# Optimization experiments

Hardware: AMD Instinct MI355X
Metric: run time of the kernel (lower is better)

The kernel has to match this reference:

```python
import jax, jax.numpy as jnp
import numpy as np

N_NODES = 200_000  # total nodes (segment id space for the CSR-style grouped reduce)


def setup_inputs() -> dict:
    key = jax.random.key(0)
    k1, k2, k3, k4, k5 = jax.random.split(key, 5)
    E, D = 1_000_000, 128   # interaction events, message dim
    B, K = 50_000, 20       # neighbor-attention batch, neighbors per node
    node_ids = jax.random.randint(k1, (E,), 0, N_NODES, dtype=jnp.int64)
    message = jax.random.normal(k2, (E, D), dtype=jnp.float32)
    timestamps = jax.random.uniform(k3, (E, 1), dtype=jnp.float32)
    nei1 = jax.random.normal(k4, (B, K, D), dtype=jnp.float32)
    nei2 = jax.random.normal(k5, (B, K, D), dtype=jnp.float32)
    return {"node_ids": node_ids, "message": message, "timestamps": timestamps,
            "nei1": nei1, "nei2": nei2}


def reference(node_ids, message, timestamps, nei1, nei2):
    # --- merged_by_segment_csr: grouped reduction over variable-length event groups.
    # torch does sort + unique_consecutive + cumsum + segment_csr; in jax the
    # equivalent (and efficient) form is a fixed-size segment reduce keyed by node id.
    ones = jnp.ones((node_ids.shape[0],), dtype=message.dtype)
    counts = jax.ops.segment_sum(ones, node_ids, num_segments=N_NODES)          # [N]
    msg_sum = jax.ops.segment_sum(message, node_ids, num_segments=N_NODES)      # [N, D]
    # msg_agg == 'mean' (segment_csr mean); empty segments yield 0.
    merged_message = msg_sum / jnp.maximum(counts, 1.0)[:, None]
    merged_t = jax.ops.segment_max(timestamps, node_ids, num_segments=N_NODES)  # [N, 1]
    merged_t = jnp.where(counts[:, None] > 0, merged_t, jnp.zeros_like(merged_t))
    # --- NeighborAttention: matmul(node1, node2^T).sum(dim=2) -> softmax over dim 0.
    # sum_j (n1[k] . n2[j]) == n1[k] . sum_j n2[j]  (avoids the [B,K,K] intermediate)
    logits = jnp.einsum('bkd,bd->bk', nei1, nei2.sum(axis=1))                   # [B, K]
    score = jax.nn.softmax(logits, axis=0)  # softmax over dim=0, as in the module
    return (merged_message, merged_t, score)
```

## Files before the change

### kernel.cpp

```cpp
#include <hip/hip_runtime.h>

#define N_NODES 200000
#define E_EVENTS 1000000
#define D_DIM 128
#define B_BATCH 50000
#define K_NEI 20

#define SCAN_BLK 196


__global__ void hist(const int* __restrict__ ids, int* __restrict__ counts)
{
    int e = blockIdx.x * blockDim.x + threadIdx.x;
    if (e < E_EVENTS) atomicAdd(counts + ids[e], 1);
}

__global__ void scan_block(const int* __restrict__ counts, int* __restrict__ blockSums)
{
    __shared__ int sd[256];
    int t = threadIdx.x, base = blockIdx.x * 1024 + t * 4;
    int s = 0;
#pragma unroll
    for (int j = 0; j < 4; ++j) { int i = base + j; if (i < N_NODES) s += counts[i]; }
    sd[t] = s; __syncthreads();
    for (int off = 128; off; off >>= 1) {
        if (t < off) sd[t] += sd[t + off];
        __syncthreads();
    }
    if (t == 0) blockSums[blockIdx.x] = sd[0];
}

__global__ void scan_tops(int* __restrict__ blockSums)
{
    __shared__ int sd[256];
    int t = threadIdx.x;
    int v = (t < SCAN_BLK) ? blockSums[t] : 0;
    sd[t] = v; __syncthreads();
    for (int off = 1; off < 256; off <<= 1) {
        int x = (t >= off) ? sd[t - off] : 0;
        __syncthreads();
        sd[t] += x;
        __syncthreads();
    }
    if (t < SCAN_BLK) blockSums[t] = sd[t] - v;
}

__global__ void scan_final(const int* __restrict__ counts, const int* __restrict__ blockSums,
                           int* __restrict__ offsets, int* __restrict__ cursor)
{
    __shared__ int sd[256];
    int t = threadIdx.x, base = blockIdx.x * 1024 + t * 4;
    int c[4];
#pragma unroll
    for (int j = 0; j < 4; ++j) { int i = base + j; c[j] = (i < N_NODES) ? counts[i] : 0; }
    int tsum = c[0] + c[1] + c[2] + c[3];
    sd[t] = tsum; __syncthreads();
    for (int off = 1; off < 256; off <<= 1) {
        int x = (t >= off) ? sd[t - off] : 0;
        __syncthreads();
        sd[t] += x;
        __syncthreads();
    }
    int excl = sd[t] - tsum + blockSums[blockIdx.x];
#pragma unroll
    for (int j = 0; j < 4; ++j) {
        int i = base + j;
        if (i < N_NODES) { offsets[i] = excl; cursor[i] = excl; }
        excl += c[j];
    }
}

template<int TSP>
__global__ void scatter_t(const int* __restrict__ ids, const float* __restrict__ ts,
                          int* __restrict__ cursor, void* __restrict__ permv)
{
    int e = blockIdx.x * blockDim.x + threadIdx.x;
    if (e < E_EVENTS) {
        int pos = atomicAdd(cursor + ids[e], 1);
        if (TSP) ((int2*)permv)[pos] = make_int2(e, __float_as_int(ts[e]));
        else     ((int*)permv)[pos]  = e;
    }
}

template<int TSP>
__global__ void __launch_bounds__(256, 8)
seg_attn_t(const void* __restrict__ permv, const int* __restrict__ offsets,
           const float* __restrict__ message, const float* __restrict__ ts,
           const float* __restrict__ nei1, const float* __restrict__ nei2,
           float* __restrict__ msg_out, float* __restrict__ t_out,
           float* __restrict__ logits)
{
    int g = blockIdx.x / 5, r = blockIdx.x % 5;
    int wid  = threadIdx.x >> 6;
    int lane = threadIdx.x & 63;
    int c = lane & 31;
    int h = lane >> 5;

    if (r < 4) {
        int n = (g * 4 + r) * 4 + wid;
        int start = offsets[n];
        int end   = (n < N_NODES - 1) ? offsets[n + 1] : E_EVENTS;
        int len   = end - start;

        const float4* msg4 = reinterpret_cast<const float4*>(message);
        float4 acc0 = make_float4(0.f, 0.f, 0.f, 0.f);
        float4 acc1 = make_float4(0.f, 0.f, 0.f, 0.f);
        float tmax = 0.f;

        for (int base = start; base < end; base += 64) {
            int cl = min(end - base, 64);
            int e_l = 0; float t_l = 0.f;
            if (lane < cl) {
                if (TSP) {
                    int2 pe = ((const int2*)permv)[base + lane];
                    e_l = pe.x; t_l = __int_as_float(pe.y);
                } else {
                    e_l = ((const int*)permv)[base + lane];
                    t_l = ts[e_l];
                }
            }
            tmax = fmaxf(tmax, t_l);
            int i = 0;
            for (; i + 8 <= cl; i += 8) {
                int eA = __shfl(e_l, i + 0 + h);
                int eB = __shfl(e_l, i + 2 + h);
                int eC = __shfl(e_l, i + 4 + h);
                int eD = __shfl(e_l, i + 6 + h);
                float4 vA = msg4[(size_t)eA * 32 + c];
                float4 vB = msg4[(size_t)eB * 32 + c];
                float4 vC = msg4[(size_t)eC * 32 + c];
                float4 vD = msg4[(size_t)eD * 32 + c];
                acc0.x += vA.x; acc0.y += vA.y; acc0.z += vA.z; acc0.w += vA.w;
                acc1.x += vB.x; acc1.y += vB.y; acc1.z += vB.z; acc1.w += vB.w;
                acc0.x += vC.x; acc0.y += vC.y; acc0.z += vC.z; acc0.w += vC.w;
                acc1.x += vD.x; acc1.y += vD.y; acc1.z += vD.z; acc1.w += vD.w;
            }
            for (; i + 2 <= cl; i += 2) {
                int e = __shfl(e_l, i + h);
                float4 v = msg4[(size_t)e * 32 + c];
                acc0.x += v.x; acc0.y += v.y; acc0.z += v.z; acc0.w += v.w;
            }
            if (i < cl) {
                int e = __shfl(e_l, i);
                if (h == 0) {
                    float4 v = msg4[(size_t)e * 32 + c];
                    acc0.x += v.x; acc0.y += v.y; acc0.z += v.z; acc0.w += v.w;
                }
            }
        }
        float4 acc = make_float4(acc0.x + acc1.x, acc0.y + acc1.y,
                                 acc0.z + acc1.z, acc0.w + acc1.w);
        acc.x += __shfl_xor(acc.x, 32);
        acc.y += __shfl_xor(acc.y, 32);
        acc.z += __shfl_xor(acc.z, 32);
        acc.w += __shfl_xor(acc.w, 32);
        float inv = 1.0f / (float)max(len, 1);
        if (h == 0) {
            reinterpret_cast<float4*>(msg_out)[(size_t)n * 32 + c] =
                make_float4(acc.x * inv, acc.y * inv, acc.z * inv, acc.w * inv);
        }
#pragma unroll
        for (int off = 32; off; off >>= 1) tmax = fmaxf(tmax, __shfl_xor(tmax, off));
        if (lane == 0) t_out[n] = tmax;
    } else {
        int b = g * 4 + wid;
        const float4* n2 = reinterpret_cast<const float4*>(nei2) + (size_t)b * (K_NEI * 32);
        float4 acc = make_float4(0.f, 0.f, 0.f, 0.f);
#pragma unroll
        for (int i = 0; i < K_NEI / 2; ++i) {
            float4 v = n2[(2 * i + h) * 32 + c];
            acc.x += v.x; acc.y += v.y; acc.z += v.z; acc.w += v.w;
        }
        float4 s4;
        s4.x = acc.x + __shfl_xor(acc.x, 32);
        s4.y = acc.y + __shfl_xor(acc.y, 32);
        s4.z = acc.z + __shfl_xor(acc.z, 32);
        s4.w = acc.w + __shfl_xor(acc.w, 32);

        const float4* n1 = reinterpret_cast<const float4*>(nei1) + (size_t)b * (K_NEI * 32);
        float p[K_NEI / 2];
#pragma unroll
        for (int i = 0; i < K_NEI / 2; ++i) {
            float4 v = n1[(2 * i + h) * 32 + c];
            float pp = v.x * s4.x + v.y * s4.y + v.z * s4.z + v.w * s4.w;
#pragma unroll
            for (int off = 16; off; off >>= 1) pp += __shfl_xor(pp, off);
            p[i] = pp;
        }
        int sel = c >> 1;
        float v = p[0];
#pragma unroll
        for (int i = 1; i < K_NEI / 2; ++i) v = (sel == i) ? p[i] : v;
        float vf = __shfl(v, ((lane & 1) << 5) + c);
        if (lane < K_NEI) logits[(size_t)b * K_NEI + lane] = vf;
    }
}

__global__ void softmax_partial(const float* __restrict__ logits, float2* __restrict__ partials)
{
    int t = threadIdx.x;
    float m[K_NEI], s[K_NEI];
#pragma unroll
    for (int k = 0; k < K_NEI; ++k) { m[k] = -INFINITY; s[k] = 0.f; }

    for (int b = blockIdx.x * 256 + t; b < B_BATCH; b += 128 * 256) {
        const float4* row = reinterpret_cast<const float4*>(logits + (size_t)b * K_NEI);
        float v[K_NEI];
#pragma unroll
        for (int q = 0; q < 5; ++q) {
            float4 rr = row[q];
            v[q * 4 + 0] = rr.x; v[q * 4 + 1] = rr.y; v[q * 4 + 2] = rr.z; v[q * 4 + 3] = rr.w;
        }
#pragma unroll
        for (int k = 0; k < K_NEI; ++k) {
            float nm = fmaxf(m[k], v[k]);
            s[k] = s[k] * expf(m[k] - nm) + expf(v[k] - nm);
            m[k] = nm;
        }
    }
#pragma unroll
    for (int k = 0; k < K_NEI; ++k) {
#pragma unroll
        for (int off = 32; off; off >>= 1) {
            float om = __shfl_xor(m[k], off);
            float os = __shfl_xor(s[k], off);
            float nm = fmaxf(m[k], om);
            s[k] = s[k] * expf(m[k] - nm) + os * expf(om - nm);
            m[k] = nm;
        }
    }
    __shared__ float lm[4][K_NEI], lsum[4][K_NEI];
    int wid = t >> 6, lane = t & 63;
    if (lane == 0) {
#pragma unroll
        for (int k = 0; k < K_NEI; ++k) { lm[wid][k] = m[k]; lsum[wid][k] = s[k]; }
    }
    __syncthreads();
    if (t < K_NEI) {
        float mm = lm[0][t], ss = lsum[0][t];
#pragma unroll
        for (int w = 1; w < 4; ++w) {
            float om = lm[w][t], os = lsum[w][t];
            float nm = fmaxf(mm, om);
            ss = ss * expf(mm - nm) + os * expf(om - nm);
            mm = nm;
        }
        partials[blockIdx.x * K_NEI + t] = make_float2(mm, ss);
    }
}

__global__ void softmax_final(const float2* __restrict__ partials, float2* __restrict__ stats)
{
    int t = threadIdx.x;
    if (t < K_NEI) {
        float mm = -INFINITY, ss = 0.f;
        for (int i = 0; i < 128; ++i) {
            float2 p = partials[i * K_NEI + t];
            float nm = fmaxf(mm, p.x);
            ss = ss * expf(mm - nm) + p.y * expf(p.x - nm);
            mm = nm;
        }
        stats[t] = make_float2(mm, ss);
    }
}

__global__ void softmax_norm(float* __restrict__ score, const float2* __restrict__ stats)
{
    int i = blockIdx.x * blockDim.x + threadIdx.x;
    if (i >= B_BATCH * K_NEI) return;
    int k = i % K_NEI;
    float2 st = stats[k];
    score[i] = expf(score[i] - st.x) / st.y;
}

extern "C" void kernel_launch(void* const* d_in, const int* in_sizes, int n_in,
                              void* d_out, int out_size, void* d_ws, size_t ws_size,
                              hipStream_t stream)
{
    const int*   node_ids = (const int*)  d_in[0];
    const float* message  = (const float*)d_in[1];
    const float* ts       = (const float*)d_in[2];
    const float* nei1     = (const float*)d_in[3];
    const float* nei2     = (const float*)d_in[4];

    float* out     = (float*)d_out;
    float* msg_out = out;
    float* t_out   = out + (size_t)N_NODES * D_DIM;
    float* score   = t_out + N_NODES;

    int*    wsi       = (int*)d_ws;
    int*    counts    = wsi;
    int*    offsets   = wsi + 200000;
    int*    cursor    = wsi + 400000;
    int*    blockSums = wsi + 600000;
    float2* stats     = (float2*)(wsi + 600256);
    float2* partials  = (float2*)(wsi + 600320);
    void*   permv     = (void*)(wsi + 605440);

    bool tsp = ws_size >= ((size_t)605440 * 4 + (size_t)E_EVENTS * 8);

    hipMemsetAsync(counts, 0, (size_t)N_NODES * sizeof(int), stream);

    hist<<<(E_EVENTS + 255) / 256, 256, 0, stream>>>(node_ids, counts);
    scan_block<<<SCAN_BLK, 256, 0, stream>>>(counts, blockSums);
    scan_tops<<<1, 256, 0, stream>>>(blockSums);
    scan_final<<<SCAN_BLK, 256, 0, stream>>>(counts, blockSums, offsets, cursor);

    if (tsp) {
        scatter_t<1><<<(E_EVENTS + 255) / 256, 256, 0, stream>>>(node_ids, ts, cursor, permv);
        seg_attn_t<1><<<12500 * 5, 256, 0, stream>>>(
            permv, offsets, message, ts, nei1, nei2, msg_out, t_out, score);
    } else {
        scatter_t<0><<<(E_EVENTS + 255) / 256, 256, 0, stream>>>(node_ids, ts, cursor, permv);
        seg_attn_t<0><<<12500 * 5, 256, 0, stream>>>(
            permv, offsets, message, ts, nei1, nei2, msg_out, t_out, score);
    }

    softmax_partial<<<128, 256, 0, stream>>>(score, partials);
    softmax_final<<<1, 64, 0, stream>>>(partials, stats);
    softmax_norm<<<(B_BATCH * K_NEI + 255) / 256, 256, 0, stream>>>(score, stats);
}
```

Baseline: 472.4 us.

## Fuse all stages into one persistent kernel with grid barriers

Replaces the chain of nine kernel launches with one persistent kernel sized to device occupancy. The stages (histogram, scan, scatter, segment reduce, attention, softmax) are separated by atomic grid-wide barriers. Part of the attention work now overlaps the scatter phase, and the segment-reduce and attention units are interleaved. This removes launch gaps and tail effects, but the grid barriers require every block to be co-resident, which risks a deadlock if occupancy is overestimated, and the fixed grid lowers parallelism in the memory-heavy phases.

```diff
diff --git a/kernel.cpp b/kernel.cpp
--- a/kernel.cpp
+++ b/kernel.cpp
@@ -6,271 +6,329 @@
 #define B_BATCH 50000
 #define K_NEI 20
 
-#define SCAN_BLK 196
-
-
-__global__ void hist(const int* __restrict__ ids, int* __restrict__ counts)
-{
-    int e = blockIdx.x * blockDim.x + threadIdx.x;
-    if (e < E_EVENTS) atomicAdd(counts + ids[e], 1);
-}
-
-__global__ void scan_block(const int* __restrict__ counts, int* __restrict__ blockSums)
-{
-    __shared__ int sd[256];
-    int t = threadIdx.x, base = blockIdx.x * 1024 + t * 4;
-    int s = 0;
-#pragma unroll
-    for (int j = 0; j < 4; ++j) { int i = base + j; if (i < N_NODES) s += counts[i]; }
-    sd[t] = s; __syncthreads();
-    for (int off = 128; off; off >>= 1) {
-        if (t < off) sd[t] += sd[t + off];
-        __syncthreads();
-    }
-    if (t == 0) blockSums[blockIdx.x] = sd[0];
-}
-
-__global__ void scan_tops(int* __restrict__ blockSums)
-{
-    __shared__ int sd[256];
-    int t = threadIdx.x;
-    int v = (t < SCAN_BLK) ? blockSums[t] : 0;
-    sd[t] = v; __syncthreads();
-    for (int off = 1; off < 256; off <<= 1) {
-        int x = (t >= off) ? sd[t - off] : 0;
-        __syncthreads();
-        sd[t] += x;
-        __syncthreads();
-    }
-    if (t < SCAN_BLK) blockSums[t] = sd[t] - v;
-}
-
-__global__ void scan_final(const int* __restrict__ counts, const int* __restrict__ blockSums,
-                           int* __restrict__ offsets, int* __restrict__ cursor)
-{
-    __shared__ int sd[256];
-    int t = threadIdx.x, base = blockIdx.x * 1024 + t * 4;
-    int c[4];
-#pragma unroll
-    for (int j = 0; j < 4; ++j) { int i = base + j; c[j] = (i < N_NODES) ? counts[i] : 0; }
-    int tsum = c[0] + c[1] + c[2] + c[3];
-    sd[t] = tsum; __syncthreads();
-    for (int off = 1; off < 256; off <<= 1) {
-        int x = (t >= off) ? sd[t - off] : 0;
-        __syncthreads();
-        sd[t] += x;
-        __syncthreads();
-    }
-    int excl = sd[t] - tsum + blockSums[blockIdx.x];
-#pragma unroll
-    for (int j = 0; j < 4; ++j) {
-        int i = base + j;
-        if (i < N_NODES) { offsets[i] = excl; cursor[i] = excl; }
-        excl += c[j];
-    }
+#define NCHUNK 196
+#define ATTN_UNITS 12500
+#define SEG_UNITS 50000
+#define ATTN_P4 2000
+
+#define WS_COUNTS   0
+#define WS_OFFSETS  200000
+#define WS_CURSOR   400000
+#define WS_CHUNK    600000
+#define WS_PARTIALS 600320
+#define WS_BARS     608256
+#define WS_PERM     608512
+
+__device__ __forceinline__ void gbar(int* bars, int idx, int G)
+{
+    __syncthreads();
+    if (threadIdx.x == 0) {
+        __threadfence();
+        __hip_atomic_fetch_add(&bars[idx * 16], 1, __ATOMIC_RELEASE,
+                               __HIP_MEMORY_SCOPE_AGENT);
+        while (__hip_atomic_load(&bars[idx * 16], __ATOMIC_ACQUIRE,
+                                 __HIP_MEMORY_SCOPE_AGENT) < G)
+            __builtin_amdgcn_s_sleep(4);
+    }
+    __syncthreads();
+}
+
+__device__ __forceinline__ void attn_unit(int u, int wid, int lane,
+    const float* __restrict__ nei1, const float* __restrict__ nei2,
+    float* __restrict__ logits)
+{
+    int b = u * 4 + wid;
+    int c = lane & 31, h = lane >> 5;
+    const float4* n2 = reinterpret_cast<const float4*>(nei2) + (size_t)b * (K_NEI * 32);
+    float4 acc = make_float4(0.f, 0.f, 0.f, 0.f);
+#pragma unroll
+    for (int i = 0; i < K_NEI / 2; ++i) {
+        float4 v = n2[(2 * i + h) * 32 + c];
+        acc.x += v.x; acc.y += v.y; acc.z += v.z; acc.w += v.w;
+    }
+    float4 s4;
+    s4.x = acc.x + __shfl_xor(acc.x, 32);
+    s4.y = acc.y + __shfl_xor(acc.y, 32);
+    s4.z = acc.z + __shfl_xor(acc.z, 32);
+    s4.w = acc.w + __shfl_xor(acc.w, 32);
+
+    const float4* n1 = reinterpret_cast<const float4*>(nei1) + (size_t)b * (K_NEI * 32);
+    float p[K_NEI / 2];
+#pragma unroll
+    for (int i = 0; i < K_NEI / 2; ++i) {
+        float4 v = n1[(2 * i + h) * 32 + c];
+        float pp = v.x * s4.x + v.y * s4.y + v.z * s4.z + v.w * s4.w;
+#pragma unroll
+        for (int off = 16; off; off >>= 1) pp += __shfl_xor(pp, off);
+        p[i] = pp;
+    }
+    int sel = c >> 1;
+    float v = p[0];
+#pragma unroll
+    for (int i = 1; i < K_NEI / 2; ++i) v = (sel == i) ? p[i] : v;
+    float vf = __shfl(v, ((lane & 1) << 5) + c);
+    if (lane < K_NEI) logits[(size_t)b * K_NEI + lane] = vf;
 }
 
 template<int TSP>
-__global__ void scatter_t(const int* __restrict__ ids, const float* __restrict__ ts,
-                          int* __restrict__ cursor, void* __restrict__ permv)
-{
-    int e = blockIdx.x * blockDim.x + threadIdx.x;
-    if (e < E_EVENTS) {
-        int pos = atomicAdd(cursor + ids[e], 1);
-        if (TSP) ((int2*)permv)[pos] = make_int2(e, __float_as_int(ts[e]));
-        else     ((int*)permv)[pos]  = e;
-    }
+__device__ __forceinline__ void seg_node(int n, int lane,
+    const void* __restrict__ permv, const int* __restrict__ offsets,
+    const float* __restrict__ message, const float* __restrict__ ts,
+    float* __restrict__ msg_out, float* __restrict__ t_out)
+{
+    int c = lane & 31, h = lane >> 5;
+    int start = offsets[n];
+    int end   = (n < N_NODES - 1) ? offsets[n + 1] : E_EVENTS;
+    int len   = end - start;
+
+    const float4* msg4 = reinterpret_cast<const float4*>(message);
+    float4 acc0 = make_float4(0.f, 0.f, 0.f, 0.f);
+    float4 acc1 = make_float4(0.f, 0.f, 0.f, 0.f);
+    float tmax = 0.f;
+
+    for (int base = start; base < end; base += 64) {
+        int cl = min(end - base, 64);
+        int e_l = 0; float t_l = 0.f;
+        if (lane < cl) {
+            if (TSP) {
+                int2 pe = ((const int2*)permv)[base + lane];
+                e_l = pe.x; t_l = __int_as_float(pe.y);
+            } else {
+                e_l = ((const int*)permv)[base + lane];
+                t_l = ts[e_l];
+            }
+        }
+        tmax = fmaxf(tmax, t_l);
+        int i = 0;
+        for (; i + 8 <= cl; i += 8) {
+            int eA = __shfl(e_l, i + 0 + h);
+            int eB = __shfl(e_l, i + 2 + h);
+            int eC = __shfl(e_l, i + 4 + h);
+            int eD = __shfl(e_l, i + 6 + h);
+            float4 vA = msg4[(size_t)eA * 32 + c];
+            float4 vB = msg4[(size_t)eB * 32 + c];
+            float4 vC = msg4[(size_t)eC * 32 + c];
+            float4 vD = msg4[(size_t)eD * 32 + c];
+            acc0.x += vA.x; acc0.y += vA.y; acc0.z += vA.z; acc0.w += vA.w;
+            acc1.x += vB.x; acc1.y += vB.y; acc1.z += vB.z; acc1.w += vB.w;
+            acc0.x += vC.x; acc0.y += vC.y; acc0.z += vC.z; acc0.w += vC.w;
+            acc1.x += vD.x; acc1.y += vD.y; acc1.z += vD.z; acc1.w += vD.w;
+        }
+        for (; i + 2 <= cl; i += 2) {
+            int e = __shfl(e_l, i + h);
+            float4 v = msg4[(size_t)e * 32 + c];
+            acc0.x += v.x; acc0.y += v.y; acc0.z += v.z; acc0.w += v.w;
+        }
+        if (i < cl) {
+            int e = __shfl(e_l, i);
+            if (h == 0) {
+                float4 v = msg4[(size_t)e * 32 + c];
+                acc0.x += v.x; acc0.y += v.y; acc0.z += v.z; acc0.w += v.w;
+            }
+        }
+    }
+    float4 acc = make_float4(acc0.x + acc1.x, acc0.y + acc1.y,
+                             acc0.z + acc1.z, acc0.w + acc1.w);
+    acc.x += __shfl_xor(acc.x, 32);
+    acc.y += __shfl_xor(acc.y, 32);
+    acc.z += __shfl_xor(acc.z, 32);
+    acc.w += __shfl_xor(acc.w, 32);
+    float inv = 1.0f / (float)max(len, 1);
+    if (h == 0) {
+        reinterpret_cast<float4*>(msg_out)[(size_t)n * 32 + c] =
+            make_float4(acc.x * inv, acc.y * inv, acc.z * inv, acc.w * inv);
+    }
+#pragma unroll
+    for (int off = 32; off; off >>= 1) tmax = fmaxf(tmax, __shfl_xor(tmax, off));
+    if (lane == 0) t_out[n] = tmax;
 }
 
 template<int TSP>
 __global__ void __launch_bounds__(256, 8)
-seg_attn_t(const void* __restrict__ permv, const int* __restrict__ offsets,
-           const float* __restrict__ message, const float* __restrict__ ts,
-           const float* __restrict__ nei1, const float* __restrict__ nei2,
-           float* __restrict__ msg_out, float* __restrict__ t_out,
-           float* __restrict__ logits)
-{
-    int g = blockIdx.x / 5, r = blockIdx.x % 5;
-    int wid  = threadIdx.x >> 6;
-    int lane = threadIdx.x & 63;
-    int c = lane & 31;
-    int h = lane >> 5;
-
-    if (r < 4) {
-        int n = (g * 4 + r) * 4 + wid;
-        int start = offsets[n];
-        int end   = (n < N_NODES - 1) ? offsets[n + 1] : E_EVENTS;
-        int len   = end - start;
-
-        const float4* msg4 = reinterpret_cast<const float4*>(message);
-        float4 acc0 = make_float4(0.f, 0.f, 0.f, 0.f);
-        float4 acc1 = make_float4(0.f, 0.f, 0.f, 0.f);
-        float tmax = 0.f;
-
-        for (int base = start; base < end; base += 64) {
-            int cl = min(end - base, 64);
-            int e_l = 0; float t_l = 0.f;
-            if (lane < cl) {
-                if (TSP) {
-                    int2 pe = ((const int2*)permv)[base + lane];
-                    e_l = pe.x; t_l = __int_as_float(pe.y);
-                } else {
-                    e_l = ((const int*)permv)[base + lane];
-                    t_l = ts[e_l];
-                }
-            }
-            tmax = fmaxf(tmax, t_l);
-            int i = 0;
-            for (; i + 8 <= cl; i += 8) {
-                int eA = __shfl(e_l, i + 0 + h);
-                int eB = __shfl(e_l, i + 2 + h);
-                int eC = __shfl(e_l, i + 4 + h);
-                int eD = __shfl(e_l, i + 6 + h);
-                float4 vA = msg4[(size_t)eA * 32 + c];
-                float4 vB = msg4[(size_t)eB * 32 + c];
-                float4 vC = msg4[(size_t)eC * 32 + c];
-                float4 vD = msg4[(size_t)eD * 32 + c];
-                acc0.x += vA.x; acc0.y += vA.y; acc0.z += vA.z; acc0.w += vA.w;
-                acc1.x += vB.x; acc1.y += vB.y; acc1.z += vB.z; acc1.w += vB.w;
-                acc0.x += vC.x; acc0.y += vC.y; acc0.z += vC.z; acc0.w += vC.w;
-                acc1.x += vD.x; acc1.y += vD.y; acc1.z += vD.z; acc1.w += vD.w;
-            }
-            for (; i + 2 <= cl; i += 2) {
-                int e = __shfl(e_l, i + h);
-                float4 v = msg4[(size_t)e * 32 + c];
-                acc0.x += v.x; acc0.y += v.y; acc0.z += v.z; acc0.w += v.w;
-            }
-            if (i < cl) {
-                int e = __shfl(e_l, i);
-                if (h == 0) {
-                    float4 v = msg4[(size_t)e * 32 + c];
-                    acc0.x += v.x; acc0.y += v.y; acc0.z += v.z; acc0.w += v.w;
-                }
-            }
-        }
-        float4 acc = make_float4(acc0.x + acc1.x, acc0.y + acc1.y,
-                                 acc0.z + acc1.z, acc0.w + acc1.w);
-        acc.x += __shfl_xor(acc.x, 32);
-        acc.y += __shfl_xor(acc.y, 32);
-        acc.z += __shfl_xor(acc.z, 32);
-        acc.w += __shfl_xor(acc.w, 32);
-        float inv = 1.0f / (float)max(len, 1);
-        if (h == 0) {
-            reinterpret_cast<float4*>(msg_out)[(size_t)n * 32 + c] =
-                make_float4(acc.x * inv, acc.y * inv, acc.z * inv, acc.w * inv);
-        }
-#pragma unroll
-        for (int off = 32; off; off >>= 1) tmax = fmaxf(tmax, __shfl_xor(tmax, off));
-        if (lane == 0) t_out[n] = tmax;
-    } else {
-        int b = g * 4 + wid;
-        const float4* n2 = reinterpret_cast<const float4*>(nei2) + (size_t)b * (K_NEI * 32);
-        float4 acc = make_float4(0.f, 0.f, 0.f, 0.f);
-#pragma unroll
-        for (int i = 0; i < K_NEI / 2; ++i) {
-            float4 v = n2[(2 * i + h) * 32 + c];
-            acc.x += v.x; acc.y += v.y; acc.z += v.z; acc.w += v.w;
-        }
-        float4 s4;
-        s4.x = acc.x + __shfl_xor(acc.x, 32);
-        s4.y = acc.y + __shfl_xor(acc.y, 32);
-        s4.z = acc.z + __shfl_xor(acc.z, 32);
-        s4.w = acc.w + __shfl_xor(acc.w, 32);
-
-        const float4* n1 = reinterpret_cast<const float4*>(nei1) + (size_t)b * (K_NEI * 32);
-        float p[K_NEI / 2];
-#pragma unroll
-        for (int i = 0; i < K_NEI / 2; ++i) {
-            float4 v = n1[(2 * i + h) * 32 + c];
-            float pp = v.x * s4.x + v.y * s4.y + v.z * s4.z + v.w * s4.w;
-#pragma unroll
-            for (int off = 16; off; off >>= 1) pp += __shfl_xor(pp, off);
-            p[i] = pp;
-        }
-        int sel = c >> 1;
-        float v = p[0];
-#pragma unroll
-        for (int i = 1; i < K_NEI / 2; ++i) v = (sel == i) ? p[i] : v;
-        float vf = __shfl(v, ((lane & 1) << 5) + c);
-        if (lane < K_NEI) logits[(size_t)b * K_NEI + lane] = vf;
-    }
-}
-
-__global__ void softmax_partial(const float* __restrict__ logits, float2* __restrict__ partials)
-{
-    int t = threadIdx.x;
-    float m[K_NEI], s[K_NEI];
-#pragma unroll
-    for (int k = 0; k < K_NEI; ++k) { m[k] = -INFINITY; s[k] = 0.f; }
-
-    for (int b = blockIdx.x * 256 + t; b < B_BATCH; b += 128 * 256) {
-        const float4* row = reinterpret_cast<const float4*>(logits + (size_t)b * K_NEI);
+mega(const int* __restrict__ ids, const float* __restrict__ message,
+     const float* __restrict__ ts,
+     const float* __restrict__ nei1, const float* __restrict__ nei2,
+     float* __restrict__ msg_out, float* __restrict__ t_out,
+     float* __restrict__ score, int* __restrict__ wsi, int G)
+{
+    int bid = blockIdx.x, t = threadIdx.x;
+    int wid = t >> 6, lane = t & 63;
+
+    int*    counts    = wsi + WS_COUNTS;
+    int*    offsets   = wsi + WS_OFFSETS;
+    int*    cursor    = wsi + WS_CURSOR;
+    int*    chunkSums = wsi + WS_CHUNK;
+    float2* partials  = (float2*)(wsi + WS_PARTIALS);
+    int*    bars      = wsi + WS_BARS;
+    void*   permv     = (void*)(wsi + WS_PERM);
+
+    __shared__ float smemf[512];
+    __shared__ int   smemi[256];
+    __shared__ float stm[K_NEI], sinv[K_NEI];
+
+    for (int e = bid * 256 + t; e < E_EVENTS; e += G * 256)
+        atomicAdd(counts + ids[e], 1);
+    gbar(bars, 0, G);
+
+    for (int cu = bid; cu < NCHUNK; cu += G) {
+        int base = cu * 1024 + t * 4, s = 0;
+#pragma unroll
+        for (int j = 0; j < 4; ++j) { int i = base + j; if (i < N_NODES) s += counts[i]; }
+        smemi[t] = s; __syncthreads();
+        for (int off = 128; off; off >>= 1) {
+            if (t < off) smemi[t] += smemi[t + off];
+            __syncthreads();
+        }
+        if (t == 0) chunkSums[cu] = smemi[0];
+        __syncthreads();
+    }
+    gbar(bars, 1, G);
+
+    if (bid == 0) {
+        int v = (t < NCHUNK) ? chunkSums[t] : 0;
+        smemi[t] = v; __syncthreads();
+        for (int off = 1; off < 256; off <<= 1) {
+            int x = (t >= off) ? smemi[t - off] : 0;
+            __syncthreads();
+            smemi[t] += x;
+            __syncthreads();
+        }
+        if (t < NCHUNK) chunkSums[t] = smemi[t] - v;
+    }
+    gbar(bars, 2, G);
+
+    for (int cu = bid; cu < NCHUNK; cu += G) {
+        int base = cu * 1024 + t * 4;
+        int c0 = (base + 0 < N_NODES) ? counts[base + 0] : 0;
+        int c1 = (base + 1 < N_NODES) ? counts[base + 1] : 0;
+        int c2 = (base + 2 < N_NODES) ? counts[base + 2] : 0;
+        int c3 = (base + 3 < N_NODES) ? counts[base + 3] : 0;
+        int tsum = c0 + c1 + c2 + c3;
+        smemi[t] = tsum; __syncthreads();
+        for (int off = 1; off < 256; off <<= 1) {
+            int x = (t >= off) ? smemi[t - off] : 0;
+            __syncthreads();
+            smemi[t] += x;
+            __syncthreads();
+        }
+        int excl = smemi[t] - tsum + chunkSums[cu];
+        if (base + 0 < N_NODES) { offsets[base + 0] = excl; cursor[base + 0] = excl; } excl += c0;
+        if (base + 1 < N_NODES) { offsets[base + 1] = excl; cursor[base + 1] = excl; } excl += c1;
+        if (base + 2 < N_NODES) { offsets[base + 2] = excl; cursor[base + 2] = excl; } excl += c2;
+        if (base + 3 < N_NODES) { offsets[base + 3] = excl; cursor[base + 3] = excl; } excl += c3;
+        __syncthreads();
+    }
+    gbar(bars, 3, G);
+
+    {
+        int Gs = G >> 1;
+        if (bid < Gs) {
+            for (int e = bid * 256 + t; e < E_EVENTS; e += Gs * 256) {
+                int pos = atomicAdd(cursor + ids[e], 1);
+                if (TSP) ((int2*)permv)[pos] = make_int2(e, __float_as_int(ts[e]));
+                else     ((int*)permv)[pos]  = e;
+            }
+        } else {
+            for (int u = bid - Gs; u < ATTN_P4; u += G - Gs)
+                attn_unit(u, wid, lane, nei1, nei2, score);
+        }
+    }
+    gbar(bars, 4, G);
+
+    for (int v = bid; v < 63000; v += G) {
+        int q = v / 6, r = v % 6;
+        if (r < 5) {
+            int s = q * 5 + r;
+            if (s < SEG_UNITS)
+                seg_node<TSP>(s * 4 + wid, lane, permv, offsets, message, ts,
+                              msg_out, t_out);
+        } else {
+            int a = ATTN_P4 + q;
+            if (a < ATTN_UNITS)
+                attn_unit(a, wid, lane, nei1, nei2, score);
+        }
+    }
+    gbar(bars, 5, G);
+
+    if (bid < NCHUNK) {
+        int b = bid * 256 + t;
+        bool val = (b < B_BATCH);
         float v[K_NEI];
-#pragma unroll
-        for (int q = 0; q < 5; ++q) {
-            float4 rr = row[q];
-            v[q * 4 + 0] = rr.x; v[q * 4 + 1] = rr.y; v[q * 4 + 2] = rr.z; v[q * 4 + 3] = rr.w;
+        if (val) {
+            const float4* row = reinterpret_cast<const float4*>(score + (size_t)b * K_NEI);
+#pragma unroll
+            for (int q = 0; q < 5; ++q) {
+                float4 r4 = row[q];
+                v[q * 4 + 0] = r4.x; v[q * 4 + 1] = r4.y;
+                v[q * 4 + 2] = r4.z; v[q * 4 + 3] = r4.w;
+            }
+        } else {
+#pragma unroll
+            for (int k = 0; k < K_NEI; ++k) v[k] = -INFINITY;
         }
 #pragma unroll
         for (int k = 0; k < K_NEI; ++k) {
-            float nm = fmaxf(m[k], v[k]);
-            s[k] = s[k] * expf(m[k] - nm) + expf(v[k] - nm);
-            m[k] = nm;
-        }
-    }
-#pragma unroll
-    for (int k = 0; k < K_NEI; ++k) {
-#pragma unroll
-        for (int off = 32; off; off >>= 1) {
-            float om = __shfl_xor(m[k], off);
-            float os = __shfl_xor(s[k], off);
-            float nm = fmaxf(m[k], om);
-            s[k] = s[k] * expf(m[k] - nm) + os * expf(om - nm);
-            m[k] = nm;
-        }
-    }
-    __shared__ float lm[4][K_NEI], lsum[4][K_NEI];
-    int wid = t >> 6, lane = t & 63;
-    if (lane == 0) {
-#pragma unroll
-        for (int k = 0; k < K_NEI; ++k) { lm[wid][k] = m[k]; lsum[wid][k] = s[k]; }
-    }
-    __syncthreads();
-    if (t < K_NEI) {
-        float mm = lm[0][t], ss = lsum[0][t];
-#pragma unroll
-        for (int w = 1; w < 4; ++w) {
-            float om = lm[w][t], os = lsum[w][t];
-            float nm = fmaxf(mm, om);
-            ss = ss * expf(mm - nm) + os * expf(om - nm);
-            mm = nm;
-        }
-        partials[blockIdx.x * K_NEI + t] = make_float2(mm, ss);
-    }
-}
-
-__global__ void softmax_final(const float2* __restrict__ partials, float2* __restrict__ stats)
-{
-    int t = threadIdx.x;
-    if (t < K_NEI) {
-        float mm = -INFINITY, ss = 0.f;
-        for (int i = 0; i < 128; ++i) {
-            float2 p = partials[i * K_NEI + t];
-            float nm = fmaxf(mm, p.x);
-            ss = ss * expf(mm - nm) + p.y * expf(p.x - nm);
-            mm = nm;
-        }
-        stats[t] = make_float2(mm, ss);
-    }
-}
-
-__global__ void softmax_norm(float* __restrict__ score, const float2* __restrict__ stats)
-{
-    int i = blockIdx.x * blockDim.x + threadIdx.x;
-    if (i >= B_BATCH * K_NEI) return;
-    int k = i % K_NEI;
-    float2 st = stats[k];
-    score[i] = expf(score[i] - st.x) / st.y;
+            float m = v[k];
+#pragma unroll
+            for (int off = 32; off; off >>= 1) m = fmaxf(m, __shfl_xor(m, off));
+            if (lane == 0) smemf[wid * K_NEI + k] = m;
+        }
+        __syncthreads();
+        float bmx[K_NEI];
+#pragma unroll
+        for (int k = 0; k < K_NEI; ++k)
+            bmx[k] = fmaxf(fmaxf(smemf[k], smemf[K_NEI + k]),
+                           fmaxf(smemf[2 * K_NEI + k], smemf[3 * K_NEI + k]));
+#pragma unroll
+        for (int k = 0; k < K_NEI; ++k) {
+            float e = val ? expf(v[k] - bmx[k]) : 0.f;
+#pragma unroll
+            for (int off = 32; off; off >>= 1) e += __shfl_xor(e, off);
+            if (lane == 0) smemf[128 + wid * K_NEI + k] = e;
+        }
+        __syncthreads();
+        if (t < K_NEI) {
+            float m4 = fmaxf(fmaxf(smemf[t], smemf[K_NEI + t]),
+                             fmaxf(smemf[2 * K_NEI + t], smemf[3 * K_NEI + t]));
+            float s4 = smemf[128 + t] + smemf[128 + K_NEI + t] +
+                       smemf[128 + 2 * K_NEI + t] + smemf[128 + 3 * K_NEI + t];
+            partials[bid * K_NEI + t] = make_float2(m4, s4);
+        }
+    }
+    gbar(bars, 6, G);
+
+    {
+        float sm = -INFINITY, ss = 0.f;
+        if (t < 240) {
+            int k = t % K_NEI;
+            int c0 = (t / K_NEI) * 17, c1 = min(c0 + 17, NCHUNK);
+            for (int j = c0; j < c1; ++j) {
+                float2 p = partials[j * K_NEI + k];
+                float nm = fmaxf(sm, p.x);
+                ss = ss * expf(sm - nm) + p.y * expf(p.x - nm);
+                sm = nm;
+            }
+        }
+        __syncthreads();
+        if (t < 240) { smemf[t] = sm; smemf[256 + t] = ss; }
+        __syncthreads();
+        if (t < K_NEI) {
+            float m = -INFINITY, s = 0.f;
+#pragma unroll
+            for (int c2 = 0; c2 < 12; ++c2) {
+                float pm = smemf[c2 * K_NEI + t], ps = smemf[256 + c2 * K_NEI + t];
+                float nm = fmaxf(m, pm);
+                s = s * expf(m - nm) + ps * expf(pm - nm);
+                m = nm;
+            }
+            stm[t] = m; sinv[t] = 1.0f / s;
+        }
+        __syncthreads();
+        for (int i = bid * 256 + t; i < B_BATCH * K_NEI; i += G * 256) {
+            int k = i % K_NEI;
+            score[i] = expf(score[i] - stm[k]) * sinv[k];
+        }
+    }
 }
 
 extern "C" void kernel_launch(void* const* d_in, const int* in_sizes, int n_in,
@@ -288,35 +346,29 @@
     float* t_out   = out + (size_t)N_NODES * D_DIM;
     float* score   = t_out + N_NODES;
 
-    int*    wsi       = (int*)d_ws;
-    int*    counts    = wsi;
-    int*    offsets   = wsi + 200000;
-    int*    cursor    = wsi + 400000;
-    int*    blockSums = wsi + 600000;
-    float2* stats     = (float2*)(wsi + 600256);
-    float2* partials  = (float2*)(wsi + 600320);
-    void*   permv     = (void*)(wsi + 605440);
-
-    bool tsp = ws_size >= ((size_t)605440 * 4 + (size_t)E_EVENTS * 8);
-
-    hipMemsetAsync(counts, 0, (size_t)N_NODES * sizeof(int), stream);
-
-    hist<<<(E_EVENTS + 255) / 256, 256, 0, stream>>>(node_ids, counts);
-    scan_block<<<SCAN_BLK, 256, 0, stream>>>(counts, blockSums);
-    scan_tops<<<1, 256, 0, stream>>>(blockSums);
-    scan_final<<<SCAN_BLK, 256, 0, stream>>>(counts, blockSums, offsets, cursor);
-
-    if (tsp) {
-        scatter_t<1><<<(E_EVENTS + 255) / 256, 256, 0, stream>>>(node_ids, ts, cursor, permv);
-        seg_attn_t<1><<<12500 * 5, 256, 0, stream>>>(
-            permv, offsets, message, ts, nei1, nei2, msg_out, t_out, score);
-    } else {
-        scatter_t<0><<<(E_EVENTS + 255) / 256, 256, 0, stream>>>(node_ids, ts, cursor, permv);
-        seg_attn_t<0><<<12500 * 5, 256, 0, stream>>>(
-            permv, offsets, message, ts, nei1, nei2, msg_out, t_out, score);
-    }
-
-    softmax_partial<<<128, 256, 0, stream>>>(score, partials);
-    softmax_final<<<1, 64, 0, stream>>>(partials, stats);
-    softmax_norm<<<(B_BATCH * K_NEI + 255) / 256, 256, 0, stream>>>(score, stats);
-}
+    int* wsi = (int*)d_ws;
+
+    bool tsp = ws_size >= ((size_t)WS_PERM + 2u * E_EVENTS) * sizeof(int);
+
+    hipMemsetAsync(wsi + WS_COUNTS, 0, (size_t)N_NODES * sizeof(int), stream);
+    hipMemsetAsync(wsi + WS_BARS,   0, 128 * sizeof(int), stream);
+
+    int numCU = 256;
+    hipDeviceGetAttribute(&numCU, hipDeviceAttributeMultiprocessorCount, 0);
+    int bpc = 0;
+    hipError_t oe;
+    if (tsp) oe = hipOccupancyMaxActiveBlocksPerMultiprocessor(
+                    &bpc, reinterpret_cast<const void*>(&mega<1>), 256, 0);
+    else     oe = hipOccupancyMaxActiveBlocksPerMultiprocessor(
+                    &bpc, reinterpret_cast<const void*>(&mega<0>), 256, 0);
+    if (oe != hipSuccess || bpc < 1) bpc = 2;
+    int G = bpc * numCU;
+    if (G > 2048) G = 2048;
+
+    if (tsp)
+        mega<1><<<G, 256, 0, stream>>>(node_ids, message, ts, nei1, nei2,
+                                       msg_out, t_out, score, wsi, G);
+    else
+        mega<0><<<G, 256, 0, stream>>>(node_ids, message, ts, nei1, nei2,
+                                       msg_out, t_out, score, wsi, G);
+}
```

After: 1.841 ms. 3.9x slower.

## Spread attention-logit work across CSR build kernels and fuse scan/softmax stages

Applied to the files above, without the earlier changes.

The attention-logit units are split across the histogram, scan and scatter kernels as extra blocks, so the bandwidth-heavy nei1/nei2 reads overlap with the latency-bound atomic and scan phases. The remainder is interleaved into the segment-reduce kernel at a 7:1 ratio. The scan-tops step is folded into the final scan, and softmax_final is merged into the normalize kernel, which cuts the launch count. Each norm block redundantly recombines all the partials. The hist and scatter kernels also switch to grid-stride loops with fewer blocks.

```diff
diff --git a/kernel.cpp b/kernel.cpp
--- a/kernel.cpp
+++ b/kernel.cpp
@@ -5,194 +5,250 @@
 #define D_DIM 128
 #define B_BATCH 50000
 #define K_NEI 20
-
-#define SCAN_BLK 196
-
-
-__global__ void hist(const int* __restrict__ ids, int* __restrict__ counts)
-{
-    int e = blockIdx.x * blockDim.x + threadIdx.x;
-    if (e < E_EVENTS) atomicAdd(counts + ids[e], 1);
-}
-
-__global__ void scan_block(const int* __restrict__ counts, int* __restrict__ blockSums)
-{
-    __shared__ int sd[256];
-    int t = threadIdx.x, base = blockIdx.x * 1024 + t * 4;
-    int s = 0;
-#pragma unroll
-    for (int j = 0; j < 4; ++j) { int i = base + j; if (i < N_NODES) s += counts[i]; }
-    sd[t] = s; __syncthreads();
-    for (int off = 128; off; off >>= 1) {
-        if (t < off) sd[t] += sd[t + off];
-        __syncthreads();
-    }
-    if (t == 0) blockSums[blockIdx.x] = sd[0];
-}
-
-__global__ void scan_tops(int* __restrict__ blockSums)
-{
-    __shared__ int sd[256];
-    int t = threadIdx.x;
-    int v = (t < SCAN_BLK) ? blockSums[t] : 0;
-    sd[t] = v; __syncthreads();
-    for (int off = 1; off < 256; off <<= 1) {
-        int x = (t >= off) ? sd[t - off] : 0;
-        __syncthreads();
-        sd[t] += x;
-        __syncthreads();
-    }
-    if (t < SCAN_BLK) blockSums[t] = sd[t] - v;
-}
-
-__global__ void scan_final(const int* __restrict__ counts, const int* __restrict__ blockSums,
-                           int* __restrict__ offsets, int* __restrict__ cursor)
-{
-    __shared__ int sd[256];
-    int t = threadIdx.x, base = blockIdx.x * 1024 + t * 4;
-    int c[4];
-#pragma unroll
-    for (int j = 0; j < 4; ++j) { int i = base + j; c[j] = (i < N_NODES) ? counts[i] : 0; }
-    int tsum = c[0] + c[1] + c[2] + c[3];
-    sd[t] = tsum; __syncthreads();
-    for (int off = 1; off < 256; off <<= 1) {
-        int x = (t >= off) ? sd[t - off] : 0;
-        __syncthreads();
-        sd[t] += x;
-        __syncthreads();
-    }
-    int excl = sd[t] - tsum + blockSums[blockIdx.x];
-#pragma unroll
-    for (int j = 0; j < 4; ++j) {
-        int i = base + j;
-        if (i < N_NODES) { offsets[i] = excl; cursor[i] = excl; }
-        excl += c[j];
-    }
+#define NCHUNK 196
+
+#define WS_COUNTS   0
+#define WS_OFFSETS  200000
+#define WS_CURSOR   400000
+#define WS_CHUNK    600000
+#define WS_PARTIALS 600320
+#define WS_PERM     605440
+
+#define A_HIST   1500
+#define A_SCANB  2100
+#define A_SCANF  2800
+#define A_SCAT   6000
+
+#define PB_HIST 512
+#define PB_SCAT 512
+
+__device__ __forceinline__ void attn_unit(int u, int wid, int lane,
+    const float* __restrict__ nei1, const float* __restrict__ nei2,
+    float* __restrict__ logits)
+{
+    int b = u * 4 + wid;
+    int c = lane & 31, h = lane >> 5;
+    const float4* n2 = reinterpret_cast<const float4*>(nei2) + (size_t)b * (K_NEI * 32);
+    float4 acc = make_float4(0.f, 0.f, 0.f, 0.f);
+#pragma unroll
+    for (int i = 0; i < K_NEI / 2; ++i) {
+        float4 v = n2[(2 * i + h) * 32 + c];
+        acc.x += v.x; acc.y += v.y; acc.z += v.z; acc.w += v.w;
+    }
+    float4 s4;
+    s4.x = acc.x + __shfl_xor(acc.x, 32);
+    s4.y = acc.y + __shfl_xor(acc.y, 32);
+    s4.z = acc.z + __shfl_xor(acc.z, 32);
+    s4.w = acc.w + __shfl_xor(acc.w, 32);
+
+    const float4* n1 = reinterpret_cast<const float4*>(nei1) + (size_t)b * (K_NEI * 32);
+    float p[K_NEI / 2];
+#pragma unroll
+    for (int i = 0; i < K_NEI / 2; ++i) {
+        float4 v = n1[(2 * i + h) * 32 + c];
+        float pp = v.x * s4.x + v.y * s4.y + v.z * s4.z + v.w * s4.w;
+#pragma unroll
+        for (int off = 16; off; off >>= 1) pp += __shfl_xor(pp, off);
+        p[i] = pp;
+    }
+    int sel = c >> 1;
+    float v = p[0];
+#pragma unroll
+    for (int i = 1; i < K_NEI / 2; ++i) v = (sel == i) ? p[i] : v;
+    float vf = __shfl(v, ((lane & 1) << 5) + c);
+    if (lane < K_NEI) logits[(size_t)b * K_NEI + lane] = vf;
 }
 
 template<int TSP>
-__global__ void scatter_t(const int* __restrict__ ids, const float* __restrict__ ts,
-                          int* __restrict__ cursor, void* __restrict__ permv)
-{
-    int e = blockIdx.x * blockDim.x + threadIdx.x;
-    if (e < E_EVENTS) {
-        int pos = atomicAdd(cursor + ids[e], 1);
-        if (TSP) ((int2*)permv)[pos] = make_int2(e, __float_as_int(ts[e]));
-        else     ((int*)permv)[pos]  = e;
-    }
-}
-
-template<int TSP>
-__global__ void __launch_bounds__(256, 8)
-seg_attn_t(const void* __restrict__ permv, const int* __restrict__ offsets,
-           const float* __restrict__ message, const float* __restrict__ ts,
-           const float* __restrict__ nei1, const float* __restrict__ nei2,
-           float* __restrict__ msg_out, float* __restrict__ t_out,
-           float* __restrict__ logits)
-{
-    int g = blockIdx.x / 5, r = blockIdx.x % 5;
-    int wid  = threadIdx.x >> 6;
-    int lane = threadIdx.x & 63;
-    int c = lane & 31;
-    int h = lane >> 5;
-
-    if (r < 4) {
-        int n = (g * 4 + r) * 4 + wid;
-        int start = offsets[n];
-        int end   = (n < N_NODES - 1) ? offsets[n + 1] : E_EVENTS;
-        int len   = end - start;
-
-        const float4* msg4 = reinterpret_cast<const float4*>(message);
-        float4 acc0 = make_float4(0.f, 0.f, 0.f, 0.f);
-        float4 acc1 = make_float4(0.f, 0.f, 0.f, 0.f);
-        float tmax = 0.f;
-
-        for (int base = start; base < end; base += 64) {
-            int cl = min(end - base, 64);
-            int e_l = 0; float t_l = 0.f;
-            if (lane < cl) {
-                if (TSP) {
-                    int2 pe = ((const int2*)permv)[base + lane];
-                    e_l = pe.x; t_l = __int_as_float(pe.y);
-                } else {
-                    e_l = ((const int*)permv)[base + lane];
-                    t_l = ts[e_l];
-                }
+__device__ __forceinline__ void seg_node(int n, int lane,
+    const void* __restrict__ permv, const int* __restrict__ offsets,
+    const float* __restrict__ message, const float* __restrict__ ts,
+    float* __restrict__ msg_out, float* __restrict__ t_out)
+{
+    int c = lane & 31, h = lane >> 5;
+    int start = offsets[n];
+    int end   = (n < N_NODES - 1) ? offsets[n + 1] : E_EVENTS;
+    int len   = end - start;
+
+    const float4* msg4 = reinterpret_cast<const float4*>(message);
+    float4 acc0 = make_float4(0.f, 0.f, 0.f, 0.f);
+    float4 acc1 = make_float4(0.f, 0.f, 0.f, 0.f);
+    float tmax = 0.f;
+
+    for (int base = start; base < end; base += 64) {
+        int cl = min(end - base, 64);
+        int e_l = 0; float t_l = 0.f;
+        if (lane < cl) {
+            if (TSP) {
+                int2 pe = ((const int2*)permv)[base + lane];
+                e_l = pe.x; t_l = __int_as_float(pe.y);
+            } else {
+                e_l = ((const int*)permv)[base + lane];
+                t_l = ts[e_l];
             }
-            tmax = fmaxf(tmax, t_l);
-            int i = 0;
-            for (; i + 8 <= cl; i += 8) {
-                int eA = __shfl(e_l, i + 0 + h);
-                int eB = __shfl(e_l, i + 2 + h);
-                int eC = __shfl(e_l, i + 4 + h);
-                int eD = __shfl(e_l, i + 6 + h);
-                float4 vA = msg4[(size_t)eA * 32 + c];
-                float4 vB = msg4[(size_t)eB * 32 + c];
-                float4 vC = msg4[(size_t)eC * 32 + c];
-                float4 vD = msg4[(size_t)eD * 32 + c];
-                acc0.x += vA.x; acc0.y += vA.y; acc0.z += vA.z; acc0.w += vA.w;
-                acc1.x += vB.x; acc1.y += vB.y; acc1.z += vB.z; acc1.w += vB.w;
-                acc0.x += vC.x; acc0.y += vC.y; acc0.z += vC.z; acc0.w += vC.w;
-                acc1.x += vD.x; acc1.y += vD.y; acc1.z += vD.z; acc1.w += vD.w;
-            }
-            for (; i + 2 <= cl; i += 2) {
-                int e = __shfl(e_l, i + h);
+        }
+        tmax = fmaxf(tmax, t_l);
+        int i = 0;
+        for (; i + 8 <= cl; i += 8) {
+            int eA = __shfl(e_l, i + 0 + h);
+            int eB = __shfl(e_l, i + 2 + h);
+            int eC = __shfl(e_l, i + 4 + h);
+            int eD = __shfl(e_l, i + 6 + h);
+            float4 vA = msg4[(size_t)eA * 32 + c];
+            float4 vB = msg4[(size_t)eB * 32 + c];
+            float4 vC = msg4[(size_t)eC * 32 + c];
+            float4 vD = msg4[(size_t)eD * 32 + c];
+            acc0.x += vA.x; acc0.y += vA.y; acc0.z += vA.z; acc0.w += vA.w;
+            acc1.x += vB.x; acc1.y += vB.y; acc1.z += vB.z; acc1.w += vB.w;
+            acc0.x += vC.x; acc0.y += vC.y; acc0.z += vC.z; acc0.w += vC.w;
+            acc1.x += vD.x; acc1.y += vD.y; acc1.z += vD.z; acc1.w += vD.w;
+        }
+        for (; i + 2 <= cl; i += 2) {
+            int e = __shfl(e_l, i + h);
+            float4 v = msg4[(size_t)e * 32 + c];
+            acc0.x += v.x; acc0.y += v.y; acc0.z += v.z; acc0.w += v.w;
+        }
+        if (i < cl) {
+            int e = __shfl(e_l, i);
+            if (h == 0) {
                 float4 v = msg4[(size_t)e * 32 + c];
                 acc0.x += v.x; acc0.y += v.y; acc0.z += v.z; acc0.w += v.w;
             }
-            if (i < cl) {
-                int e = __shfl(e_l, i);
-                if (h == 0) {
-                    float4 v = msg4[(size_t)e * 32 + c];
-                    acc0.x += v.x; acc0.y += v.y; acc0.z += v.z; acc0.w += v.w;
-                }
-            }
-        }
-        float4 acc = make_float4(acc0.x + acc1.x, acc0.y + acc1.y,
-                                 acc0.z + acc1.z, acc0.w + acc1.w);
-        acc.x += __shfl_xor(acc.x, 32);
-        acc.y += __shfl_xor(acc.y, 32);
-        acc.z += __shfl_xor(acc.z, 32);
-        acc.w += __shfl_xor(acc.w, 32);
-        float inv = 1.0f / (float)max(len, 1);
-        if (h == 0) {
-            reinterpret_cast<float4*>(msg_out)[(size_t)n * 32 + c] =
-                make_float4(acc.x * inv, acc.y * inv, acc.z * inv, acc.w * inv);
-        }
-#pragma unroll
-        for (int off = 32; off; off >>= 1) tmax = fmaxf(tmax, __shfl_xor(tmax, off));
-        if (lane == 0) t_out[n] = tmax;
-    } else {
-        int b = g * 4 + wid;
-        const float4* n2 = reinterpret_cast<const float4*>(nei2) + (size_t)b * (K_NEI * 32);
-        float4 acc = make_float4(0.f, 0.f, 0.f, 0.f);
-#pragma unroll
-        for (int i = 0; i < K_NEI / 2; ++i) {
-            float4 v = n2[(2 * i + h) * 32 + c];
-            acc.x += v.x; acc.y += v.y; acc.z += v.z; acc.w += v.w;
-        }
-        float4 s4;
-        s4.x = acc.x + __shfl_xor(acc.x, 32);
-        s4.y = acc.y + __shfl_xor(acc.y, 32);
-        s4.z = acc.z + __shfl_xor(acc.z, 32);
-        s4.w = acc.w + __shfl_xor(acc.w, 32);
-
-        const float4* n1 = reinterpret_cast<const float4*>(nei1) + (size_t)b * (K_NEI * 32);
-        float p[K_NEI / 2];
-#pragma unroll
-        for (int i = 0; i < K_NEI / 2; ++i) {
-            float4 v = n1[(2 * i + h) * 32 + c];
-            float pp = v.x * s4.x + v.y * s4.y + v.z * s4.z + v.w * s4.w;
-#pragma unroll
-            for (int off = 16; off; off >>= 1) pp += __shfl_xor(pp, off);
-            p[i] = pp;
-        }
-        int sel = c >> 1;
-        float v = p[0];
-#pragma unroll
-        for (int i = 1; i < K_NEI / 2; ++i) v = (sel == i) ? p[i] : v;
-        float vf = __shfl(v, ((lane & 1) << 5) + c);
-        if (lane < K_NEI) logits[(size_t)b * K_NEI + lane] = vf;
+        }
+    }
+    float4 acc = make_float4(acc0.x + acc1.x, acc0.y + acc1.y,
+                             acc0.z + acc1.z, acc0.w + acc1.w);
+    acc.x += __shfl_xor(acc.x, 32);
+    acc.y += __shfl_xor(acc.y, 32);
+    acc.z += __shfl_xor(acc.z, 32);
+    acc.w += __shfl_xor(acc.w, 32);
+    float inv = 1.0f / (float)max(len, 1);
+    if (h == 0) {
+        reinterpret_cast<float4*>(msg_out)[(size_t)n * 32 + c] =
+            make_float4(acc.x * inv, acc.y * inv, acc.z * inv, acc.w * inv);
+    }
+#pragma unroll
+    for (int off = 32; off; off >>= 1) tmax = fmaxf(tmax, __shfl_xor(tmax, off));
+    if (lane == 0) t_out[n] = tmax;
+}
+
+__global__ void __launch_bounds__(256)
+k_hist(const int* __restrict__ ids, int* __restrict__ counts,
+       const float* __restrict__ nei1, const float* __restrict__ nei2,
+       float* __restrict__ score)
+{
+    int bid = blockIdx.x, t = threadIdx.x;
+    if (bid < PB_HIST) {
+        for (int e = bid * 256 + t; e < E_EVENTS; e += PB_HIST * 256)
+            atomicAdd(counts + ids[e], 1);
+    } else {
+        attn_unit(bid - PB_HIST, t >> 6, t & 63, nei1, nei2, score);
+    }
+}
+
+__global__ void __launch_bounds__(256)
+k_scanb(const int* __restrict__ counts, int* __restrict__ chunkSums,
+        const float* __restrict__ nei1, const float* __restrict__ nei2,
+        float* __restrict__ score)
+{
+    int bid = blockIdx.x, t = threadIdx.x;
+    if (bid < NCHUNK) {
+        __shared__ int sd[256];
+        int base = bid * 1024 + t * 4, s = 0;
+#pragma unroll
+        for (int j = 0; j < 4; ++j) { int i = base + j; if (i < N_NODES) s += counts[i]; }
+        sd[t] = s; __syncthreads();
+        for (int off = 128; off; off >>= 1) {
+            if (t < off) sd[t] += sd[t + off];
+            __syncthreads();
+        }
+        if (t == 0) chunkSums[bid] = sd[0];
+    } else {
+        attn_unit(A_HIST + (bid - NCHUNK), t >> 6, t & 63, nei1, nei2, score);
+    }
+}
+
+__global__ void __launch_bounds__(256)
+k_scanf(const int* __restrict__ counts, const int* __restrict__ chunkSums,
+        int* __restrict__ offsets, int* __restrict__ cursor,
+        const float* __restrict__ nei1, const float* __restrict__ nei2,
+        float* __restrict__ score)
+{
+    int bid = blockIdx.x, t = threadIdx.x;
+    if (bid < NCHUNK) {
+        __shared__ int sd[256];
+        int v = (t < NCHUNK) ? chunkSums[t] : 0;
+        sd[t] = v; __syncthreads();
+        for (int off = 1; off < 256; off <<= 1) {
+            int x = (t >= off) ? sd[t - off] : 0;
+            __syncthreads();
+            sd[t] += x;
+            __syncthreads();
+        }
+        int chunkBase = (bid == 0) ? 0 : sd[bid - 1];
+        __syncthreads();
+        int base = bid * 1024 + t * 4;
+        int c0 = (base + 0 < N_NODES) ? counts[base + 0] : 0;
+        int c1 = (base + 1 < N_NODES) ? counts[base + 1] : 0;
+        int c2 = (base + 2 < N_NODES) ? counts[base + 2] : 0;
+        int c3 = (base + 3 < N_NODES) ? counts[base + 3] : 0;
+        int tsum = c0 + c1 + c2 + c3;
+        sd[t] = tsum; __syncthreads();
+        for (int off = 1; off < 256; off <<= 1) {
+            int x = (t >= off) ? sd[t - off] : 0;
+            __syncthreads();
+            sd[t] += x;
+            __syncthreads();
+        }
+        int excl = sd[t] - tsum + chunkBase;
+        if (base + 0 < N_NODES) { offsets[base + 0] = excl; cursor[base + 0] = excl; } excl += c0;
+        if (base + 1 < N_NODES) { offsets[base + 1] = excl; cursor[base + 1] = excl; } excl += c1;
+        if (base + 2 < N_NODES) { offsets[base + 2] = excl; cursor[base + 2] = excl; } excl += c2;
+        if (base + 3 < N_NODES) { offsets[base + 3] = excl; cursor[base + 3] = excl; } excl += c3;
+    } else {
+        attn_unit(A_SCANB + (bid - NCHUNK), t >> 6, t & 63, nei1, nei2, score);
+    }
+}
+
+template<int TSP>
+__global__ void __launch_bounds__(256)
+k_scat(const int* __restrict__ ids, const float* __restrict__ ts,
+       int* __restrict__ cursor, void* __restrict__ permv,
+       const float* __restrict__ nei1, const float* __restrict__ nei2,
+       float* __restrict__ score)
+{
+    int bid = blockIdx.x, t = threadIdx.x;
+    if (bid < PB_SCAT) {
+        for (int e = bid * 256 + t; e < E_EVENTS; e += PB_SCAT * 256) {
+            int pos = atomicAdd(cursor + ids[e], 1);
+            if (TSP) ((int2*)permv)[pos] = make_int2(e, __float_as_int(ts[e]));
+            else     ((int*)permv)[pos]  = e;
+        }
+    } else {
+        attn_unit(A_SCANF + (bid - PB_SCAT), t >> 6, t & 63, nei1, nei2, score);
+    }
+}
+
+template<int TSP>
+__global__ void __launch_bounds__(256, 8)
+k_seg(const void* __restrict__ permv, const int* __restrict__ offsets,
+      const float* __restrict__ message, const float* __restrict__ ts,
+      const float* __restrict__ nei1, const float* __restrict__ nei2,
+      float* __restrict__ msg_out, float* __restrict__ t_out,
+      float* __restrict__ score)
+{
+    int v = blockIdx.x, t = threadIdx.x;
+    int q = v >> 3, r = v & 7;
+    int wid = t >> 6, lane = t & 63;
+    if (r < 7) {
+        int s = q * 7 + r;
+        if (s < 50000)
+            seg_node<TSP>(s * 4 + wid, lane, permv, offsets, message, ts,
+                          msg_out, t_out);
+    } else {
+        int u = A_SCAT + q;
+        if (u < 12500)
+            attn_unit(u, wid, lane, nei1, nei2, score);
     }
 }
 
@@ -249,28 +305,41 @@
     }
 }
 
-__global__ void softmax_final(const float2* __restrict__ partials, float2* __restrict__ stats)
-{
+__global__ void __launch_bounds__(256)
+k_norm(float* __restrict__ score, const float2* __restrict__ partials)
+{
+    __shared__ float sm[256], ssum[256];
+    __shared__ float stm[K_NEI], sinv[K_NEI];
     int t = threadIdx.x;
+    float m = -INFINITY, s = 0.f;
+    if (t < 240) {
+        int k = t % K_NEI, g = t / K_NEI;
+        int j0 = g * 11, j1 = min(j0 + 11, 128);
+        for (int j = j0; j < j1; ++j) {
+            float2 p = partials[j * K_NEI + k];
+            float nm = fmaxf(m, p.x);
+            s = s * expf(m - nm) + p.y * expf(p.x - nm);
+            m = nm;
+        }
+    }
+    sm[t] = m; ssum[t] = s; __syncthreads();
     if (t < K_NEI) {
         float mm = -INFINITY, ss = 0.f;
-        for (int i = 0; i < 128; ++i) {
-            float2 p = partials[i * K_NEI + t];
-            float nm = fmaxf(mm, p.x);
-            ss = ss * expf(mm - nm) + p.y * expf(p.x - nm);
+#pragma unroll
+        for (int g = 0; g < 12; ++g) {
+            float pm = sm[g * K_NEI + t], ps = ssum[g * K_NEI + t];
+            float nm = fmaxf(mm, pm);
+            ss = ss * expf(mm - nm) + ps * expf(pm - nm);
             mm = nm;
         }
-        stats[t] = make_float2(mm, ss);
-    }
-}
-
-__global__ void softmax_norm(float* __restrict__ score, const float2* __restrict__ stats)
-{
-    int i = blockIdx.x * blockDim.x + threadIdx.x;
-    if (i >= B_BATCH * K_NEI) return;
-    int k = i % K_NEI;
-    float2 st = stats[k];
-    score[i] = expf(score[i] - st.x) / st.y;
+        stm[t] = mm; sinv[t] = 1.0f / ss;
+    }
+    __syncthreads();
+    int i = blockIdx.x * 256 + t;
+    if (i < B_BATCH * K_NEI) {
+        int k = i % K_NEI;
+        score[i] = expf(score[i] - stm[k]) * sinv[k];
+    }
 }
 
 extern "C" void kernel_launch(void* const* d_in, const int* in_sizes, int n_in,
@@ -289,34 +358,33 @@
     float* score   = t_out + N_NODES;
 
     int*    wsi       = (int*)d_ws;
-    int*    counts    = wsi;
-    int*    offsets   = wsi + 200000;
-    int*    cursor    = wsi + 400000;
-    int*    blockSums = wsi + 600000;
-    float2* stats     = (float2*)(wsi + 600256);
-    float2* partials  = (float2*)(wsi + 600320);
-    void*   permv     = (void*)(wsi + 605440);
-
-    bool tsp = ws_size >= ((size_t)605440 * 4 + (size_t)E_EVENTS * 8);
+    int*    counts    = wsi + WS_COUNTS;
+    int*    offsets   = wsi + WS_OFFSETS;
+    int*    cursor    = wsi + WS_CURSOR;
+    int*    chunkSums = wsi + WS_CHUNK;
+    float2* partials  = (float2*)(wsi + WS_PARTIALS);
+    void*   permv     = (void*)(wsi + WS_PERM);
+
+    bool tsp = ws_size >= ((size_t)WS_PERM + 2u * E_EVENTS) * sizeof(int);
 
     hipMemsetAsync(counts, 0, (size_t)N_NODES * sizeof(int), stream);
 
-    hist<<<(E_EVENTS + 255) / 256, 256, 0, stream>>>(node_ids, counts);
-    scan_block<<<SCAN_BLK, 256, 0, stream>>>(counts, blockSums);
-    scan_tops<<<1, 256, 0, stream>>>(blockSums);
-    scan_final<<<SCAN_BLK, 256, 0, stream>>>(counts, blockSums, offsets, cursor);
-
+    k_hist<<<PB_HIST + A_HIST, 256, 0, stream>>>(node_ids, counts, nei1, nei2, score);
+    k_scanb<<<NCHUNK + (A_SCANB - A_HIST), 256, 0, stream>>>(counts, chunkSums, nei1, nei2, score);
+    k_scanf<<<NCHUNK + (A_SCANF - A_SCANB), 256, 0, stream>>>(counts, chunkSums, offsets, cursor,
+                                                              nei1, nei2, score);
     if (tsp) {
-        scatter_t<1><<<(E_EVENTS + 255) / 256, 256, 0, stream>>>(node_ids, ts, cursor, permv);
-        seg_attn_t<1><<<12500 * 5, 256, 0, stream>>>(
+        k_scat<1><<<PB_SCAT + (A_SCAT - A_SCANF), 256, 0, stream>>>(
+            node_ids, ts, cursor, permv, nei1, nei2, score);
+        k_seg<1><<<57144, 256, 0, stream>>>(
             permv, offsets, message, ts, nei1, nei2, msg_out, t_out, score);
     } else {
-        scatter_t<0><<<(E_EVENTS + 255) / 256, 256, 0, stream>>>(node_ids, ts, cursor, permv);
-        seg_attn_t<0><<<12500 * 5, 256, 0, stream>>>(
+        k_scat<0><<<PB_SCAT + (A_SCAT - A_SCANF), 256, 0, stream>>>(
+            node_ids, ts, cursor, permv, nei1, nei2, score);
+        k_seg<0><<<57144, 256, 0, stream>>>(
             permv, offsets, message, ts, nei1, nei2, msg_out, t_out, score);
     }
 
     softmax_partial<<<128, 256, 0, stream>>>(score, partials);
-    softmax_final<<<1, 64, 0, stream>>>(partials, stats);
-    softmax_norm<<<(B_BATCH * K_NEI + 255) / 256, 256, 0, stream>>>(score, stats);
-}
+    k_norm<<<(B_BATCH * K_NEI + 255) / 256, 256, 0, stream>>>(score, partials);
+}
```

Measured after the change: 624.8 us. +32.3%, slower.
